# Performance work log

Measured on AMD Instinct MI355X. Metric: run time of the kernel, lower is better.

The kernel has to match this reference:

```python
import jax, jax.numpy as jnp
import numpy as np

N_NODES = 100000
N_EDGES = 1600000
N_GRAPHS = 64
D_IN = 3
HIDDEN = 256
N_CLASSES = 10
NEG_SLOPE = 0.01  # torch F.leaky_relu default


def gcn_conv(x, W, b, src, dst, n_nodes):
    """GCNConv: D^{-1/2}(A+I)D^{-1/2} X W + b with self-loops."""
    h = x @ W  # [N, H]
    ones = jnp.ones(src.shape[0], h.dtype)
    deg = jax.ops.segment_sum(ones, dst, num_segments=n_nodes) + 1.0  # +1 self-loop
    dinv = jax.lax.rsqrt(deg)
    coef = dinv[src] * dinv[dst]  # [E]
    agg = jax.ops.segment_sum(h[src] * coef[:, None], dst, num_segments=n_nodes)
    agg = agg + h * (1.0 / deg)[:, None]  # self-loop contribution (norm = 1/deg)
    return agg + b


def leaky_relu(v):
    return jnp.where(v >= 0, v, NEG_SLOPE * v)


def setup_inputs() -> dict:
    key = jax.random.key(0)
    ks = jax.random.split(key, 12)
    x = jax.random.normal(ks[0], (N_NODES, D_IN), dtype=jnp.float32)
    edge_index = jax.random.randint(ks[1], (2, N_EDGES), 0, N_NODES, dtype=jnp.int32)
    batch = jnp.sort(jax.random.randint(ks[2], (N_NODES,), 0, N_GRAPHS, dtype=jnp.int32))
    s1 = 1.0 / np.sqrt(D_IN)
    s2 = 1.0 / np.sqrt(HIDDEN)
    W1 = jax.random.uniform(ks[3], (D_IN, HIDDEN), jnp.float32, -s1, s1)
    b1 = jnp.zeros((HIDDEN,), jnp.float32)
    W2 = jax.random.uniform(ks[4], (HIDDEN, HIDDEN), jnp.float32, -s2, s2)
    b2 = jnp.zeros((HIDDEN,), jnp.float32)
    W3 = jax.random.uniform(ks[5], (HIDDEN, HIDDEN), jnp.float32, -s2, s2)
    b3 = jnp.zeros((HIDDEN,), jnp.float32)
    Wc = jax.random.uniform(ks[6], (HIDDEN, N_CLASSES), jnp.float32, -s2, s2)
    bc = jax.random.uniform(ks[7], (N_CLASSES,), jnp.float32, -s2, s2)
    return {"x": x, "edge_index": edge_index, "batch": batch,
            "W1": W1, "b1": b1, "W2": W2, "b2": b2, "W3": W3, "b3": b3,
            "Wc": Wc, "bc": bc}


def reference(x, edge_index, batch, W1, b1, W2, b2, W3, b3, Wc, bc):
    src, dst = edge_index[0], edge_index[1]
    h = leaky_relu(gcn_conv(x, W1, b1, src, dst, N_NODES))
    h = leaky_relu(gcn_conv(h, W2, b2, src, dst, N_NODES))
    h = leaky_relu(gcn_conv(h, W3, b3, src, dst, N_NODES))
    # global mean pool over graphs
    sums = jax.ops.segment_sum(h, batch, num_segments=N_GRAPHS)
    cnt = jax.ops.segment_sum(jnp.ones((N_NODES,), h.dtype), batch, num_segments=N_GRAPHS)
    pooled = sums / jnp.maximum(cnt, 1.0)[:, None]  # [G, H]
    logits = pooled @ Wc + bc
    return jax.nn.softmax(logits, axis=1)
```

## Files before the change

kernel.cpp:

```cpp
#include <hip/hip_runtime.h>
#include <hip/hip_bf16.h>
#include <hip/hip_fp16.h>
#include <cstdint>
#include <cstddef>

#define N_NODES   100000
#define N_EDGES   1600000
#define N_GRAPHS  64
#define HIDDEN    256
#define N_CLASSES 10
#define NEG_SLOPE 0.01f

#define E_PAD    (N_EDGES + 8 * N_NODES)
#define GEMM_BLOCKS 391
#define SLICE_SZ ((size_t)N_NODES * 32)

#define PART_EDGES  8192
#define PART_BLOCKS ((N_EDGES + PART_EDGES - 1) / PART_EDGES)
#define SUB_BITS 10
#define SUB_SIZE 1024
#define N_SUB    ((N_NODES + SUB_SIZE - 1) / SUB_SIZE)
#define CAP_SUB  17408

typedef __attribute__((ext_vector_type(4))) float f32x4;
typedef __attribute__((ext_vector_type(2))) float f32x2;

__device__ __forceinline__ float bf2f(unsigned short u) {
    return __uint_as_float(((unsigned int)u) << 16);
}

__device__ __forceinline__ unsigned char f2fp8(float v) {
    return (unsigned char)(__builtin_amdgcn_cvt_pk_fp8_f32(v, v, 0, false) & 0xff);
}

__device__ __forceinline__ unsigned int rec_pack(int s, float c) {
    __half h = __float2half(c);
    unsigned short hb = reinterpret_cast<const __half_raw*>(&h)->x;
    return ((unsigned int)hb << 17) | (unsigned int)s;
}
__device__ __forceinline__ float rec_coef(unsigned int u) {
    __half_raw hr; hr.x = (unsigned short)(u >> 17);
    return __half2float(*reinterpret_cast<const __half*>(&hr));
}

__global__ __launch_bounds__(256) void k_partition(const int* __restrict__ src, const int* __restrict__ dst,
                                                   int* __restrict__ gcur, unsigned int* __restrict__ bucket) {
    __shared__ int lcnt[N_SUB];
    __shared__ int lbase[N_SUB];
    __shared__ int gbase[N_SUB];
    __shared__ unsigned int stage[PART_EDGES];
    int tid = threadIdx.x;
    for (int i = tid; i < N_SUB; i += 256) lcnt[i] = 0;
    __syncthreads();
    int e0 = blockIdx.x * PART_EDGES + tid * 8;
    for (int g = 0; g < 4; ++g) {
        int e = e0 + g * 2048;
        if (e < N_EDGES) {
            int4 da = *(const int4*)(dst + e);
            int4 db = *(const int4*)(dst + e + 4);
            int d[8] = {da.x, da.y, da.z, da.w, db.x, db.y, db.z, db.w};
#pragma unroll
            for (int j = 0; j < 8; ++j) atomicAdd(&lcnt[d[j] >> SUB_BITS], 1);
        }
    }
    __syncthreads();
    if (tid == 0) {
        int s = 0;
        for (int r = 0; r < N_SUB; ++r) { lbase[r] = s; s += lcnt[r]; }
    }
    __syncthreads();
    for (int i = tid; i < N_SUB; i += 256) {
        gbase[i] = atomicAdd(&gcur[i * 16], lcnt[i]);
        lcnt[i] = lbase[i];
    }
    __syncthreads();
    for (int g = 0; g < 4; ++g) {
        int e = e0 + g * 2048;
        if (e < N_EDGES) {
            int4 da = *(const int4*)(dst + e);
            int4 db = *(const int4*)(dst + e + 4);
            int4 sa = *(const int4*)(src + e);
            int4 sb = *(const int4*)(src + e + 4);
            int d[8] = {da.x, da.y, da.z, da.w, db.x, db.y, db.z, db.w};
            int s[8] = {sa.x, sa.y, sa.z, sa.w, sb.x, sb.y, sb.z, sb.w};
#pragma unroll
            for (int j = 0; j < 8; ++j) {
                int r = d[j] >> SUB_BITS;
                int p = atomicAdd(&lcnt[r], 1);
                stage[p] = ((unsigned int)(d[j] & (SUB_SIZE - 1)) << 17) | (unsigned int)s[j];
            }
        }
    }
    __syncthreads();
    int wv = tid >> 6, ln = tid & 63;
    for (int r = wv; r < N_SUB; r += 4) {
        int base = lbase[r], n = lcnt[r] - base, gb = gbase[r];
        unsigned int* dp = bucket + (size_t)r * CAP_SUB + gb;
        for (int k = ln; k < n; k += 64) dp[k] = stage[base + k];
    }
}

__global__ __launch_bounds__(512) void k_hist3(const unsigned int* __restrict__ bucket,
                                               const int* __restrict__ gcur, int* __restrict__ cnt,
                                               const float* __restrict__ x,
                                               float* __restrict__ dinv, float4* __restrict__ xp) {
    int sub = blockIdx.x;
    __shared__ int hist[SUB_SIZE];
    for (int i = threadIdx.x; i < SUB_SIZE; i += 512) hist[i] = 0;
    __syncthreads();
    int n = gcur[sub * 16];
    const unsigned int* bp = bucket + (size_t)sub * CAP_SUB;
    for (int i0 = threadIdx.x * 8; i0 < n; i0 += 512 * 8) {
        uint4 ua = *(const uint4*)(bp + i0);
        uint4 ub = *(const uint4*)(bp + i0 + 4);
        unsigned int u[8] = {ua.x, ua.y, ua.z, ua.w, ub.x, ub.y, ub.z, ub.w};
        int m = n - i0; if (m > 8) m = 8;
#pragma unroll
        for (int j = 0; j < 8; ++j) if (j < m) atomicAdd(&hist[u[j] >> 17], 1);
    }
    __syncthreads();
    int base = sub * SUB_SIZE;
    for (int i = threadIdx.x; i < SUB_SIZE; i += 512) {
        int node = base + i;
        if (node < N_NODES) {
            int c = hist[i];
            cnt[node] = c;
            dinv[node] = rsqrtf((float)c + 1.0f);
            xp[node] = make_float4(x[node * 3 + 0], x[node * 3 + 1], x[node * 3 + 2], 0.f);
        }
    }
}

__global__ __launch_bounds__(512) void k_fill3(const unsigned int* __restrict__ bucket,
                                               const int* __restrict__ gcur,
                                               const float* __restrict__ dinv,
                                               const int* __restrict__ off,
                                               unsigned int* __restrict__ rec) {
    int sub = blockIdx.x;
    __shared__ int lcur[SUB_SIZE];
    __shared__ float ldv[SUB_SIZE];
    int nb0 = sub * SUB_SIZE;
    for (int i = threadIdx.x; i < SUB_SIZE; i += 512) {
        int node = nb0 + i;
        lcur[i] = (node < N_NODES) ? off[node] : 0;
        ldv[i]  = (node < N_NODES) ? dinv[node] : 0.f;
    }
    __syncthreads();
    int n = gcur[sub * 16];
    const unsigned int* bp = bucket + (size_t)sub * CAP_SUB;
    for (int i0 = threadIdx.x * 8; i0 < n; i0 += 512 * 8) {
        uint4 ua = *(const uint4*)(bp + i0);
        uint4 ub = *(const uint4*)(bp + i0 + 4);
        unsigned int u[8] = {ua.x, ua.y, ua.z, ua.w, ub.x, ub.y, ub.z, ub.w};
        int m = n - i0; if (m > 8) m = 8;
        float ds[8];
#pragma unroll
        for (int j = 0; j < 8; ++j) {
            int s = (j < m) ? (int)(u[j] & 0x1ffff) : 0;
            ds[j] = dinv[s];
        }
#pragma unroll
        for (int j = 0; j < 8; ++j) {
            if (j < m) {
                int dr = (int)(u[j] >> 17);
                float c = ds[j] * ldv[dr];
                int p = atomicAdd(&lcur[dr], 1);
                rec[p] = rec_pack((int)(u[j] & 0x1ffff), c);
            }
        }
    }
}

__global__ void k_graph_bounds(const int* __restrict__ batch,
                               int* __restrict__ gstart, int* __restrict__ gcnt) {
    int g = threadIdx.x;
    int lo = 0, hi = N_NODES;
    while (lo < hi) { int mid = (lo + hi) >> 1; if (batch[mid] < g) lo = mid + 1; else hi = mid; }
    __shared__ int sh[N_GRAPHS + 1];
    sh[g] = lo;
    if (g == 0) sh[N_GRAPHS] = N_NODES;
    __syncthreads();
    gstart[g] = sh[g];
    gcnt[g]   = sh[g + 1] - sh[g];
}

__global__ void k_scanA(const int* __restrict__ cnt, int* __restrict__ out, int* __restrict__ bsum) {
    __shared__ int sh[256];
    int tid = threadIdx.x;
    int base = blockIdx.x * 1024 + tid * 4;
    int v[4]; int s = 0;
#pragma unroll
    for (int i = 0; i < 4; i++) {
        int idx = base + i;
        v[i] = (idx < N_NODES) ? ((cnt[idx] + 7) & ~7) : 0;
        s += v[i];
    }
    sh[tid] = s; __syncthreads();
    for (int off = 1; off < 256; off <<= 1) {
        int t = (tid >= off) ? sh[tid - off] : 0;
        __syncthreads();
        sh[tid] += t;
        __syncthreads();
    }
    int excl = sh[tid] - s;
    if (tid == 255) bsum[blockIdx.x] = sh[255];
#pragma unroll
    for (int i = 0; i < 4; i++) { int idx = base + i; if (idx < N_NODES) out[idx] = excl; excl += v[i]; }
}

__global__ void k_scanB(int* __restrict__ bsum, int nb) {
    __shared__ int sh[128];
    int tid = threadIdx.x;
    int v = (tid < nb) ? bsum[tid] : 0;
    sh[tid] = v; __syncthreads();
    for (int off = 1; off < 128; off <<= 1) {
        int t = (tid >= off) ? sh[tid - off] : 0;
        __syncthreads();
        sh[tid] += t;
        __syncthreads();
    }
    if (tid < nb) bsum[tid] = sh[tid] - v;
}

__global__ void k_scanC(int* __restrict__ off_arr, const int* __restrict__ bsum,
                        const int* __restrict__ cnt, unsigned int* __restrict__ rec) {
    int i = blockIdx.x * 256 + threadIdx.x;
    if (i < N_NODES) {
        int v = off_arr[i] + bsum[i >> 10];
        off_arr[i] = v;
        int c  = cnt[i];
        int cp = (c + 7) & ~7;
        for (int p = v + c; p < v + cp; ++p) rec[p] = 0u;
        if (i == N_NODES - 1) off_arr[N_NODES] = v + cp;
    }
}

__global__ void k_wprep(const float* __restrict__ W, unsigned char* __restrict__ Wswz) {
    int n = blockIdx.x; int k = threadIdx.x;
    unsigned char v = f2fp8(W[k * HIDDEN + n]);
    int k0 = k >> 5, nt = n >> 4;
    int lane = (((k >> 3) & 3) << 4) | (n & 15);
    int j = k & 7;
    Wswz[(size_t)(((k0 * 16) + nt) * 64 + lane) * 8 + j] = v;
}

__global__ void k_agg3(const float4* __restrict__ xp, const int* __restrict__ off,
                       const unsigned int* __restrict__ rec, const float* __restrict__ dinv,
                       float4* __restrict__ ax) {
    int i = blockIdx.x * 256 + threadIdx.x;
    if (i >= N_NODES) return;
    float di = dinv[i];
    float selfc = di * di;
    float4 xi = xp[i];
    float a0 = xi.x * selfc, a1 = xi.y * selfc, a2 = xi.z * selfc;
    int e = off[i], e1 = off[i + 1];
    for (; e < e1; e += 4) {
        uint4 rr = *(const uint4*)(rec + e);
        int s0 = rr.x & 0x1ffff, s1 = rr.y & 0x1ffff, s2 = rr.z & 0x1ffff, s3 = rr.w & 0x1ffff;
        float c0 = rec_coef(rr.x), c1 = rec_coef(rr.y), c2 = rec_coef(rr.z), c3 = rec_coef(rr.w);
        float4 x0 = xp[s0], x1 = xp[s1], x2 = xp[s2], x3 = xp[s3];
        a0 += c0 * x0.x + c1 * x1.x + c2 * x2.x + c3 * x3.x;
        a1 += c0 * x0.y + c1 * x1.y + c2 * x2.y + c3 * x3.y;
        a2 += c0 * x0.z + c1 * x1.z + c2 * x2.z + c3 * x3.z;
    }
    ax[i] = make_float4(a0, a1, a2, 0.f);
}

__global__ __launch_bounds__(256) void k_l1(const float4* __restrict__ ax, const float* __restrict__ W1,
                                            const float* __restrict__ b1, unsigned char* __restrict__ out) {
    __shared__ float w0s[HIDDEN], w1s[HIDDEN], w2s[HIDDEN], bbs[HIDDEN];
    int t = threadIdx.x;
    w0s[t] = W1[t]; w1s[t] = W1[HIDDEN + t]; w2s[t] = W1[2 * HIDDEN + t]; bbs[t] = b1[t];
    __syncthreads();
    int base = blockIdx.x * 32;
#pragma unroll 4
    for (int i = 0; i < 32; ++i) {
        int node = base + i;
        if (node >= N_NODES) break;
        float4 a = ax[node];
        float v = a.x * w0s[t] + a.y * w1s[t] + a.z * w2s[t] + bbs[t];
        v = v >= 0.f ? v : NEG_SLOPE * v;
        out[(size_t)node * HIDDEN + t] = f2fp8(v);
    }
}

__global__ __launch_bounds__(512, 2) void k_gemm_mfma(const unsigned char* __restrict__ A,
                                                      const unsigned char* __restrict__ Wswz,
                                                      unsigned char* __restrict__ C, int M) {
    __shared__ long Bs[8192];
    __shared__ unsigned int St[8][320];
    int tid = threadIdx.x;
    {
        const float4* gsrc = (const float4*)Wswz;
        float4* ldst = (float4*)Bs;
#pragma unroll
        for (int i = 0; i < 8; ++i) ldst[tid + 512 * i] = gsrc[tid + 512 * i];
    }
    __syncthreads();
    int lane = tid & 63, wv = tid >> 6;
    int quad = lane >> 4, r = lane & 15;
    int nstrips = M >> 4;
    unsigned int* stw = &St[wv][0];
    int rrow = lane >> 2, rseg = lane & 3;
    for (int s = blockIdx.x * 8 + wv; s < nstrips; s += GEMM_BLOCKS * 8) {
        int m0 = s * 16;
        const long* Ab = (const long*)(A + (size_t)(m0 + r) * HIDDEN) + quad;
        long af[8];
#pragma unroll
        for (int k0 = 0; k0 < 8; ++k0) af[k0] = Ab[k0 * 4];
        f32x4 acc[16];
#pragma unroll
        for (int i = 0; i < 16; i++) acc[i] = (f32x4){0.f, 0.f, 0.f, 0.f};
#pragma unroll
        for (int k0 = 0; k0 < 8; ++k0) {
#pragma unroll
            for (int nt = 0; nt < 16; ++nt) {
                long w = Bs[(k0 * 16 + nt) * 64 + lane];
                acc[nt] = __builtin_amdgcn_mfma_f32_16x16x32_fp8_fp8(w, af[k0], acc[nt], 0, 0, 0);
            }
        }
#pragma unroll
        for (int q4 = 0; q4 < 4; ++q4) {
#pragma unroll
            for (int t = 0; t < 4; ++t) {
                f32x4 a = acc[q4 * 4 + t];
                unsigned int pk = __builtin_amdgcn_cvt_pk_fp8_f32(a[0], a[1], 0, false);
                pk = __builtin_amdgcn_cvt_pk_fp8_f32(a[2], a[3], pk, true);
                stw[r * 20 + t * 4 + quad] = pk;
            }
            uint4 v = *(const uint4*)&stw[rrow * 20 + rseg * 4];
            int slice = 2 * q4 + (rseg >> 1);
            *(uint4*)(C + (size_t)slice * SLICE_SZ + (size_t)(m0 + rrow) * 32 + (rseg & 1) * 16) = v;
        }
    }
}

__global__ __launch_bounds__(256) void k_agg(const unsigned char* __restrict__ h,
                                             const float* __restrict__ bias,
                                             const int* __restrict__ off, const unsigned int* __restrict__ rec,
                                             const float* __restrict__ dinv,
                                             unsigned char* __restrict__ out) {
    int slice = blockIdx.x & 7;
    int node = (blockIdx.x >> 3) * 32 + (threadIdx.x >> 3);
    int sl = threadIdx.x & 7;
    const unsigned char* hs = h + (size_t)slice * SLICE_SZ + sl * 4;
    float di = dinv[node];
    float selfc = di * di;
    unsigned int hv = *(const unsigned int*)(hs + (size_t)node * 32);
    f32x2 hlo = __builtin_amdgcn_cvt_pk_f32_fp8(hv, false);
    f32x2 hhi = __builtin_amdgcn_cvt_pk_f32_fp8(hv, true);
    float4 bv = *(const float4*)(bias + slice * 32 + sl * 4);
    float a0 = bv.x + hlo.x * selfc, a1 = bv.y + hlo.y * selfc;
    float a2 = bv.z + hhi.x * selfc, a3 = bv.w + hhi.y * selfc;
    int e = off[node], e1 = off[node + 1];
    for (; e < e1; e += 8) {
        uint4 ra = *(const uint4*)(rec + e);
        uint4 rb = *(const uint4*)(rec + e + 4);
        unsigned int w0 = *(const unsigned int*)(hs + (size_t)(ra.x & 0x1ffff) * 32);
        unsigned int w1 = *(const unsigned int*)(hs + (size_t)(ra.y & 0x1ffff) * 32);
        unsigned int w2 = *(const unsigned int*)(hs + (size_t)(ra.z & 0x1ffff) * 32);
        unsigned int w3 = *(const unsigned int*)(hs + (size_t)(ra.w & 0x1ffff) * 32);
        unsigned int w4 = *(const unsigned int*)(hs + (size_t)(rb.x & 0x1ffff) * 32);
        unsigned int w5 = *(const unsigned int*)(hs + (size_t)(rb.y & 0x1ffff) * 32);
        unsigned int w6 = *(const unsigned int*)(hs + (size_t)(rb.z & 0x1ffff) * 32);
        unsigned int w7 = *(const unsigned int*)(hs + (size_t)(rb.w & 0x1ffff) * 32);
        float c0 = rec_coef(ra.x), c1 = rec_coef(ra.y), c2 = rec_coef(ra.z), c3 = rec_coef(ra.w);
        float c4 = rec_coef(rb.x), c5 = rec_coef(rb.y), c6 = rec_coef(rb.z), c7 = rec_coef(rb.w);
        f32x2 l0 = __builtin_amdgcn_cvt_pk_f32_fp8(w0, false), g0 = __builtin_amdgcn_cvt_pk_f32_fp8(w0, true);
        f32x2 l1 = __builtin_amdgcn_cvt_pk_f32_fp8(w1, false), g1 = __builtin_amdgcn_cvt_pk_f32_fp8(w1, true);
        f32x2 l2 = __builtin_amdgcn_cvt_pk_f32_fp8(w2, false), g2 = __builtin_amdgcn_cvt_pk_f32_fp8(w2, true);
        f32x2 l3 = __builtin_amdgcn_cvt_pk_f32_fp8(w3, false), g3 = __builtin_amdgcn_cvt_pk_f32_fp8(w3, true);
        f32x2 l4 = __builtin_amdgcn_cvt_pk_f32_fp8(w4, false), g4 = __builtin_amdgcn_cvt_pk_f32_fp8(w4, true);
        f32x2 l5 = __builtin_amdgcn_cvt_pk_f32_fp8(w5, false), g5 = __builtin_amdgcn_cvt_pk_f32_fp8(w5, true);
        f32x2 l6 = __builtin_amdgcn_cvt_pk_f32_fp8(w6, false), g6 = __builtin_amdgcn_cvt_pk_f32_fp8(w6, true);
        f32x2 l7 = __builtin_amdgcn_cvt_pk_f32_fp8(w7, false), g7 = __builtin_amdgcn_cvt_pk_f32_fp8(w7, true);
        a0 += c0 * l0.x + c1 * l1.x + c2 * l2.x + c3 * l3.x
            + c4 * l4.x + c5 * l5.x + c6 * l6.x + c7 * l7.x;
        a1 += c0 * l0.y + c1 * l1.y + c2 * l2.y + c3 * l3.y
            + c4 * l4.y + c5 * l5.y + c6 * l6.y + c7 * l7.y;
        a2 += c0 * g0.x + c1 * g1.x + c2 * g2.x + c3 * g3.x
            + c4 * g4.x + c5 * g5.x + c6 * g6.x + c7 * g7.x;
        a3 += c0 * g0.y + c1 * g1.y + c2 * g2.y + c3 * g3.y
            + c4 * g4.y + c5 * g5.y + c6 * g6.y + c7 * g7.y;
    }
    a0 = a0 >= 0.f ? a0 : NEG_SLOPE * a0;
    a1 = a1 >= 0.f ? a1 : NEG_SLOPE * a1;
    a2 = a2 >= 0.f ? a2 : NEG_SLOPE * a2;
    a3 = a3 >= 0.f ? a3 : NEG_SLOPE * a3;
    unsigned int pk = __builtin_amdgcn_cvt_pk_fp8_f32(a0, a1, 0, false);
    pk = __builtin_amdgcn_cvt_pk_fp8_f32(a2, a3, pk, true);
    *(unsigned int*)(out + (size_t)node * HIDDEN + slice * 32 + sl * 4) = pk;
}

__global__ void k_pool(const unsigned char* __restrict__ h, const int* __restrict__ gstart,
                       const int* __restrict__ gcnt, float* __restrict__ pooled) {
    int g = blockIdx.x, chunk = blockIdx.y, t = threadIdx.x;
    int s = gstart[g], c = gcnt[g];
    int i0 = s + (int)(((long long)c * chunk) / 16);
    int i1 = s + (int)(((long long)c * (chunk + 1)) / 16);
    float acc = 0.f;
    for (int i = i0; i < i1; ++i) {
        f32x2 v = __builtin_amdgcn_cvt_pk_f32_fp8((unsigned int)h[(size_t)i * HIDDEN + t], false);
        acc += v.x;
    }
    atomicAdd(&pooled[g * HIDDEN + t], acc);
}

__global__ void k_head(const float* __restrict__ pooled, const int* __restrict__ gcnt,
                       const float* __restrict__ Wc, const float* __restrict__ bc,
                       float* __restrict__ out) {
    int g = blockIdx.x; int l = threadIdx.x;
    float inv = 1.0f / fmaxf((float)gcnt[g], 1.0f);
    float p[4];
#pragma unroll
    for (int i = 0; i < 4; i++) p[i] = pooled[g * HIDDEN + l + i * 64] * inv;
    __shared__ float logits[N_CLASSES];
#pragma unroll
    for (int j = 0; j < N_CLASSES; j++) {
        float s = 0.f;
#pragma unroll
        for (int i = 0; i < 4; i++) s += p[i] * Wc[(l + i * 64) * N_CLASSES + j];
        for (int o = 32; o > 0; o >>= 1) s += __shfl_down(s, o, 64);
        if (l == 0) logits[j] = s + bc[j];
    }
    __syncthreads();
    if (l == 0) {
        float m = logits[0];
        for (int j = 1; j < N_CLASSES; j++) m = fmaxf(m, logits[j]);
        float e[N_CLASSES]; float sum = 0.f;
        for (int j = 0; j < N_CLASSES; j++) { e[j] = expf(logits[j] - m); sum += e[j]; }
        for (int j = 0; j < N_CLASSES; j++) out[g * N_CLASSES + j] = e[j] / sum;
    }
}

extern "C" void kernel_launch(void* const* d_in, const int* in_sizes, int n_in,
                              void* d_out, int out_size, void* d_ws, size_t ws_size,
                              hipStream_t stream) {
    const float* x     = (const float*)d_in[0];
    const int*   edge  = (const int*)d_in[1];
    const int*   batch = (const int*)d_in[2];
    const float* W1 = (const float*)d_in[3];
    const float* b1 = (const float*)d_in[4];
    const float* W2 = (const float*)d_in[5];
    const float* b2 = (const float*)d_in[6];
    const float* W3 = (const float*)d_in[7];
    const float* b3 = (const float*)d_in[8];
    const float* Wc = (const float*)d_in[9];
    const float* bc = (const float*)d_in[10];
    float* out = (float*)d_out;
    const int* srcp = edge;
    const int* dstp = edge + N_EDGES;

    char* ws = (char*)d_ws;
    size_t off = 0;
    auto alloc = [&](size_t bytes) -> char* {
        char* p = ws + off;
        off += (bytes + 255) & ~(size_t)255;
        return p;
    };
    unsigned char* hA   = (unsigned char*)alloc((size_t)N_NODES * HIDDEN);
    unsigned char* hB   = (unsigned char*)alloc((size_t)N_NODES * HIDDEN);
    unsigned char* Wz2  = (unsigned char*)alloc((size_t)HIDDEN * HIDDEN);
    unsigned char* Wz3  = (unsigned char*)alloc((size_t)HIDDEN * HIDDEN);
    int*   deg_cnt  = (int*)alloc((size_t)N_NODES * 4);
    float* dinv     = (float*)alloc((size_t)N_NODES * 4);
    int*   csr_off  = (int*)alloc((size_t)(N_NODES + 1) * 4);
    unsigned int* csr_rec = (unsigned int*)alloc((size_t)E_PAD * 4);
    float4* ax      = (float4*)alloc((size_t)N_NODES * 16);
    float4* xp      = (float4*)alloc((size_t)N_NODES * 16);
    int*   gcnt     = (int*)alloc((size_t)N_GRAPHS * 4);
    int*   gstart   = (int*)alloc((size_t)N_GRAPHS * 4);
    float* pooled   = (float*)alloc((size_t)N_GRAPHS * HIDDEN * 4);
    int*   bsum     = (int*)alloc(128 * 4);
    int*   gcur     = (int*)alloc((size_t)N_SUB * 16 * 4);

    unsigned int* bucket = (unsigned int*)hB;

    hipMemsetAsync(gcur, 0, (size_t)N_SUB * 16 * 4, stream);
    hipMemsetAsync(pooled, 0, (size_t)N_GRAPHS * HIDDEN * 4, stream);

    int nb  = (N_NODES + 255) / 256;
    int sblocks = (N_NODES + 1023) / 1024;

    k_partition<<<PART_BLOCKS, 256, 0, stream>>>(srcp, dstp, gcur, bucket);
    k_graph_bounds<<<1, 64, 0, stream>>>(batch, gstart, gcnt);
    k_hist3<<<N_SUB, 512, 0, stream>>>(bucket, gcur, deg_cnt, x, dinv, xp);
    k_scanA<<<sblocks, 256, 0, stream>>>(deg_cnt, csr_off, bsum);
    k_scanB<<<1, 128, 0, stream>>>(bsum, sblocks);
    k_scanC<<<nb, 256, 0, stream>>>(csr_off, bsum, deg_cnt, csr_rec);
    k_fill3<<<N_SUB, 512, 0, stream>>>(bucket, gcur, dinv, csr_off, csr_rec);
    k_wprep<<<HIDDEN, HIDDEN, 0, stream>>>(W2, Wz2);
    k_wprep<<<HIDDEN, HIDDEN, 0, stream>>>(W3, Wz3);

    k_agg3<<<nb, 256, 0, stream>>>(xp, csr_off, csr_rec, dinv, ax);
    k_l1<<<(N_NODES + 31) / 32, 256, 0, stream>>>(ax, W1, b1, hA);

    int aggb = ((N_NODES + 31) / 32) * 8;
    k_gemm_mfma<<<GEMM_BLOCKS, 512, 0, stream>>>(hA, Wz2, hB, N_NODES);
    k_agg<<<aggb, 256, 0, stream>>>(hB, b2, csr_off, csr_rec, dinv, hA);
    k_gemm_mfma<<<GEMM_BLOCKS, 512, 0, stream>>>(hA, Wz3, hB, N_NODES);
    k_agg<<<aggb, 256, 0, stream>>>(hB, b3, csr_off, csr_rec, dinv, hA);
    dim3 pg(N_GRAPHS, 16);
    k_pool<<<pg, 256, 0, stream>>>(hA, gstart, gcnt, pooled);
    k_head<<<N_GRAPHS, 64, 0, stream>>>(pooled, gcnt, Wc, bc, out);
}
```

Before: 481.9 us.

## Degree-sort nodes per block for aggregation and use sliced feature layout throughout

Adds a per-1024-node counting sort by degree that produces a permutation, so each aggregation wavefront processes nodes of similar degree and lane divergence from uneven edge loops shrinks. The layer-1 output, GEMM A-operand reads, aggregation output and pooling now all use the 8-slice, 32-byte-per-node layout the GEMM already wrote, so aggregation writes are per-slice contiguous. The cost is an extra kernel plus a perm lookup, scattered output writes in permuted order, and strided GEMM A loads across slices.

Result: no change. 483.5 us (+0.3%).

```diff
diff --git a/kernel.cpp b/kernel.cpp
--- a/kernel.cpp
+++ b/kernel.cpp
@@ -129,6 +129,35 @@
             xp[node] = make_float4(x[node * 3 + 0], x[node * 3 + 1], x[node * 3 + 2], 0.f);
         }
     }
+}
+
+__global__ __launch_bounds__(512) void k_locsort(const int* __restrict__ cnt, int* __restrict__ perm) {
+    int sub = blockIdx.x, t = threadIdx.x;
+    __shared__ int hist[256];
+    __shared__ int curs[256];
+    if (t < 256) hist[t] = 0;
+    __syncthreads();
+    int base = sub * SUB_SIZE;
+    int i0 = base + t, i1 = base + t + 512;
+    int d0 = -1, d1 = -1;
+    if (i0 < N_NODES) { d0 = min(cnt[i0], 254); atomicAdd(&hist[d0], 1); }
+    if (i1 < N_NODES) { d1 = min(cnt[i1], 254); atomicAdd(&hist[d1], 1); }
+    __syncthreads();
+    if (t < 256) curs[t] = hist[t];
+    __syncthreads();
+    for (int off = 1; off < 256; off <<= 1) {
+        int v = 0;
+        if (t < 256 && t >= off) v = curs[t - off];
+        __syncthreads();
+        if (t < 256) curs[t] += v;
+        __syncthreads();
+    }
+    if (t < 256) curs[t] -= hist[t];
+    __syncthreads();
+    if (d0 >= 0) { int p = atomicAdd(&curs[d0], 1); perm[base + p] = i0; }
+    if (d1 >= 0) { int p = atomicAdd(&curs[d1], 1); perm[base + p] = i1; }
+    int nvalid = N_NODES - base; if (nvalid > SUB_SIZE) nvalid = SUB_SIZE;
+    for (int k = nvalid + t; k < SUB_SIZE; k += 512) perm[base + k] = 0x7fffffff;
 }
 
 __global__ __launch_bounds__(512) void k_fill3(const unsigned int* __restrict__ bucket,
@@ -273,6 +302,7 @@
     w0s[t] = W1[t]; w1s[t] = W1[HIDDEN + t]; w2s[t] = W1[2 * HIDDEN + t]; bbs[t] = b1[t];
     __syncthreads();
     int base = blockIdx.x * 32;
+    size_t obase = (size_t)(t >> 5) * SLICE_SZ + (t & 31);
 #pragma unroll 4
     for (int i = 0; i < 32; ++i) {
         int node = base + i;
@@ -280,7 +310,7 @@
         float4 a = ax[node];
         float v = a.x * w0s[t] + a.y * w1s[t] + a.z * w2s[t] + bbs[t];
         v = v >= 0.f ? v : NEG_SLOPE * v;
-        out[(size_t)node * HIDDEN + t] = f2fp8(v);
+        out[obase + (size_t)node * 32] = f2fp8(v);
     }
 }
 
@@ -304,10 +334,10 @@
     int rrow = lane >> 2, rseg = lane & 3;
     for (int s = blockIdx.x * 8 + wv; s < nstrips; s += GEMM_BLOCKS * 8) {
         int m0 = s * 16;
-        const long* Ab = (const long*)(A + (size_t)(m0 + r) * HIDDEN) + quad;
+        const unsigned char* Abase = A + (size_t)(m0 + r) * 32 + quad * 8;
         long af[8];
 #pragma unroll
-        for (int k0 = 0; k0 < 8; ++k0) af[k0] = Ab[k0 * 4];
+        for (int k0 = 0; k0 < 8; ++k0) af[k0] = *(const long*)(Abase + (size_t)k0 * SLICE_SZ);
         f32x4 acc[16];
 #pragma unroll
         for (int i = 0; i < 16; i++) acc[i] = (f32x4){0.f, 0.f, 0.f, 0.f};
@@ -339,31 +369,36 @@
                                              const float* __restrict__ bias,
                                              const int* __restrict__ off, const unsigned int* __restrict__ rec,
                                              const float* __restrict__ dinv,
+                                             const int* __restrict__ perm,
                                              unsigned char* __restrict__ out) {
     int slice = blockIdx.x & 7;
-    int node = (blockIdx.x >> 3) * 32 + (threadIdx.x >> 3);
-    int sl = threadIdx.x & 7;
-    const unsigned char* hs = h + (size_t)slice * SLICE_SZ + sl * 4;
-    float di = dinv[node];
+    int gi = (blockIdx.x >> 3) * 32 + (threadIdx.x >> 3);
+    unsigned sl4 = (threadIdx.x & 7) * 4;
+    int node = perm[gi];
+    bool valid = node < N_NODES;
+    int nd = valid ? node : 0;
+    const unsigned char* hsl = h + (size_t)slice * SLICE_SZ;
+    float di = dinv[nd];
     float selfc = di * di;
-    unsigned int hv = *(const unsigned int*)(hs + (size_t)node * 32);
+    unsigned int hv = *(const unsigned int*)(hsl + ((unsigned)nd << 5) + sl4);
     f32x2 hlo = __builtin_amdgcn_cvt_pk_f32_fp8(hv, false);
     f32x2 hhi = __builtin_amdgcn_cvt_pk_f32_fp8(hv, true);
-    float4 bv = *(const float4*)(bias + slice * 32 + sl * 4);
+    float4 bv = *(const float4*)(bias + slice * 32 + (threadIdx.x & 7) * 4);
     float a0 = bv.x + hlo.x * selfc, a1 = bv.y + hlo.y * selfc;
     float a2 = bv.z + hhi.x * selfc, a3 = bv.w + hhi.y * selfc;
-    int e = off[node], e1 = off[node + 1];
+    int e = valid ? off[nd] : 0;
+    int e1 = valid ? off[nd + 1] : 0;
     for (; e < e1; e += 8) {
         uint4 ra = *(const uint4*)(rec + e);
         uint4 rb = *(const uint4*)(rec + e + 4);
-        unsigned int w0 = *(const unsigned int*)(hs + (size_t)(ra.x & 0x1ffff) * 32);
-        unsigned int w1 = *(const unsigned int*)(hs + (size_t)(ra.y & 0x1ffff) * 32);
-        unsigned int w2 = *(const unsigned int*)(hs + (size_t)(ra.z & 0x1ffff) * 32);
-        unsigned int w3 = *(const unsigned int*)(hs + (size_t)(ra.w & 0x1ffff) * 32);
-        unsigned int w4 = *(const unsigned int*)(hs + (size_t)(rb.x & 0x1ffff) * 32);
-        unsigned int w5 = *(const unsigned int*)(hs + (size_t)(rb.y & 0x1ffff) * 32);
-        unsigned int w6 = *(const unsigned int*)(hs + (size_t)(rb.z & 0x1ffff) * 32);
-        unsigned int w7 = *(const unsigned int*)(hs + (size_t)(rb.w & 0x1ffff) * 32);
+        unsigned int w0 = *(const unsigned int*)(hsl + ((ra.x & 0x1ffffu) << 5) + sl4);
+        unsigned int w1 = *(const unsigned int*)(hsl + ((ra.y & 0x1ffffu) << 5) + sl4);
+        unsigned int w2 = *(const unsigned int*)(hsl + ((ra.z & 0x1ffffu) << 5) + sl4);
+        unsigned int w3 = *(const unsigned int*)(hsl + ((ra.w & 0x1ffffu) << 5) + sl4);
+        unsigned int w4 = *(const unsigned int*)(hsl + ((rb.x & 0x1ffffu) << 5) + sl4);
+        unsigned int w5 = *(const unsigned int*)(hsl + ((rb.y & 0x1ffffu) << 5) + sl4);
+        unsigned int w6 = *(const unsigned int*)(hsl + ((rb.z & 0x1ffffu) << 5) + sl4);
+        unsigned int w7 = *(const unsigned int*)(hsl + ((rb.w & 0x1ffffu) << 5) + sl4);
         float c0 = rec_coef(ra.x), c1 = rec_coef(ra.y), c2 = rec_coef(ra.z), c3 = rec_coef(ra.w);
         float c4 = rec_coef(rb.x), c5 = rec_coef(rb.y), c6 = rec_coef(rb.z), c7 = rec_coef(rb.w);
         f32x2 l0 = __builtin_amdgcn_cvt_pk_f32_fp8(w0, false), g0 = __builtin_amdgcn_cvt_pk_f32_fp8(w0, true);
@@ -389,7 +424,8 @@
     a3 = a3 >= 0.f ? a3 : NEG_SLOPE * a3;
     unsigned int pk = __builtin_amdgcn_cvt_pk_fp8_f32(a0, a1, 0, false);
     pk = __builtin_amdgcn_cvt_pk_fp8_f32(a2, a3, pk, true);
-    *(unsigned int*)(out + (size_t)node * HIDDEN + slice * 32 + sl * 4) = pk;
+    if (valid)
+        *(unsigned int*)(out + (size_t)slice * SLICE_SZ + ((unsigned)nd << 5) + sl4) = pk;
 }
 
 __global__ void k_pool(const unsigned char* __restrict__ h, const int* __restrict__ gstart,
@@ -398,9 +434,10 @@
     int s = gstart[g], c = gcnt[g];
     int i0 = s + (int)(((long long)c * chunk) / 16);
     int i1 = s + (int)(((long long)c * (chunk + 1)) / 16);
+    const unsigned char* hs = h + (size_t)(t >> 5) * SLICE_SZ + (t & 31);
     float acc = 0.f;
     for (int i = i0; i < i1; ++i) {
-        f32x2 v = __builtin_amdgcn_cvt_pk_f32_fp8((unsigned int)h[(size_t)i * HIDDEN + t], false);
+        f32x2 v = __builtin_amdgcn_cvt_pk_f32_fp8((unsigned int)hs[(size_t)i * 32], false);
         acc += v.x;
     }
     atomicAdd(&pooled[g * HIDDEN + t], acc);
@@ -473,6 +510,7 @@
     float* pooled   = (float*)alloc((size_t)N_GRAPHS * HIDDEN * 4);
     int*   bsum     = (int*)alloc(128 * 4);
     int*   gcur     = (int*)alloc((size_t)N_SUB * 16 * 4);
+    int*   perm     = (int*)alloc((size_t)N_SUB * SUB_SIZE * 4);
 
     unsigned int* bucket = (unsigned int*)hB;
 
@@ -485,6 +523,7 @@
     k_partition<<<PART_BLOCKS, 256, 0, stream>>>(srcp, dstp, gcur, bucket);
     k_graph_bounds<<<1, 64, 0, stream>>>(batch, gstart, gcnt);
     k_hist3<<<N_SUB, 512, 0, stream>>>(bucket, gcur, deg_cnt, x, dinv, xp);
+    k_locsort<<<N_SUB, 512, 0, stream>>>(deg_cnt, perm);
     k_scanA<<<sblocks, 256, 0, stream>>>(deg_cnt, csr_off, bsum);
     k_scanB<<<1, 128, 0, stream>>>(bsum, sblocks);
     k_scanC<<<nb, 256, 0, stream>>>(csr_off, bsum, deg_cnt, csr_rec);
@@ -495,11 +534,11 @@
     k_agg3<<<nb, 256, 0, stream>>>(xp, csr_off, csr_rec, dinv, ax);
     k_l1<<<(N_NODES + 31) / 32, 256, 0, stream>>>(ax, W1, b1, hA);
 
-    int aggb = ((N_NODES + 31) / 32) * 8;
+    int aggb = (N_SUB * SUB_SIZE / 32) * 8;
     k_gemm_mfma<<<GEMM_BLOCKS, 512, 0, stream>>>(hA, Wz2, hB, N_NODES);
-    k_agg<<<aggb, 256, 0, stream>>>(hB, b2, csr_off, csr_rec, dinv, hA);
+    k_agg<<<aggb, 256, 0, stream>>>(hB, b2, csr_off, csr_rec, dinv, perm, hA);
     k_gemm_mfma<<<GEMM_BLOCKS, 512, 0, stream>>>(hA, Wz3, hB, N_NODES);
-    k_agg<<<aggb, 256, 0, stream>>>(hB, b3, csr_off, csr_rec, dinv, hA);
+    k_agg<<<aggb, 256, 0, stream>>>(hB, b3, csr_off, csr_rec, dinv, perm, hA);
     dim3 pg(N_GRAPHS, 16);
     k_pool<<<pg, 256, 0, stream>>>(hA, gstart, gcnt, pooled);
     k_head<<<N_GRAPHS, 64, 0, stream>>>(pooled, gcnt, Wc, bc, out);
```
